# Performance work log

Hardware: AMD Instinct MI355X
Metric: run time of the kernel (lower is better)

## Reference

```python
import jax, jax.numpy as jnp
import numpy as np

B, C, T, H, HB, E, EH, TH = 512, 30, 3, 512, 512, 6, 512, 512
SCALE = 0.02
LOSS_COEF = 0.01


def setup_inputs() -> dict:
    key = jax.random.key(0)
    ks = jax.random.split(key, 12)
    return {
        "candidate_cls_embed": jax.random.normal(ks[0], (B, C, H), jnp.float32),
        "scores": jax.random.uniform(ks[1], (B, T, C), dtype=jnp.float32),
        "fc1_w": jax.random.normal(ks[2], (H, HB), jnp.float32) * SCALE,
        "fc1_b": jnp.zeros((HB,), jnp.float32),
        "fc2_w": jax.random.normal(ks[3], (HB, H), jnp.float32) * SCALE,
        "fc2_b": jnp.zeros((H,), jnp.float32),
        "w_gate": jax.random.normal(ks[4], (T, H, E), jnp.float32) * SCALE,
        "expert_w1": jax.random.normal(ks[5], (E, H, EH), jnp.float32) * SCALE,
        "expert_b1": jnp.zeros((E, EH), jnp.float32),
        "expert_w2": jax.random.normal(ks[6], (E, EH, H), jnp.float32) * SCALE,
        "expert_b2": jnp.zeros((E, H), jnp.float32),
        "tower_w1": jax.random.normal(ks[7], (T, H, TH), jnp.float32) * SCALE,
        "tower_b1": jnp.zeros((T, TH), jnp.float32),
        "tower_w2": jax.random.normal(ks[8], (T, TH), jnp.float32) * SCALE,
        "tower_b2": jnp.zeros((T,), jnp.float32),
        "k": 3,
    }


def reference(candidate_cls_embed, scores, fc1_w, fc1_b, fc2_w, fc2_b, w_gate,
              expert_w1, expert_b1, expert_w2, expert_b2,
              tower_w1, tower_b1, tower_w2, tower_b2, k):
    n_experts = w_gate.shape[-1]
    n_tasks = scores.shape[1]

    # labels: 1 where score hits the per-task max (non-differentiable construction)
    labels = jax.lax.stop_gradient(
        (scores == scores.max(axis=-1, keepdims=True)).astype(scores.dtype))  # [B,T,C]

    # shared bottom: fc2(relu(fc1(x)))
    h = jax.nn.relu(candidate_cls_embed @ fc1_w + fc1_b) @ fc2_w + fc2_b  # [B,C,H]

    # per-task top-k gating (MMoE style)
    glog = jnp.einsum('bch,the->btce', h, w_gate)                 # [B,T,C,E]
    topv, topi = jax.lax.top_k(glog, k)                           # [B,T,C,k]
    topg = jax.nn.softmax(topv, axis=-1)                          # softmax over kept experts
    gates = jnp.sum(topg[..., None] * jax.nn.one_hot(topi, n_experts, dtype=topg.dtype),
                    axis=-2)                                      # [B,T,C,E]

    # all-expert MLPs (dense over E; E is small)
    eh = jax.nn.relu(jnp.einsum('bch,ehf->bcef', h, expert_w1) + expert_b1)  # [B,C,E,EH]
    eo = jnp.einsum('bcef,efh->bceh', eh, expert_w2) + expert_b2             # [B,C,E,H]

    # gated combination per task
    y = jnp.einsum('btce,bceh->btch', gates, eo)                  # [B,T,C,H]

    # per-task towers -> one logit per candidate
    th = jax.nn.relu(jnp.einsum('btch,thf->btcf', y, tower_w1) + tower_b1[None, :, None, :])
    logits = jnp.einsum('btcf,tf->btc', th, tower_w2) + tower_b2[None, :, None]  # [B,T,C]

    # BCE-with-logits, mean over candidates, mean over tasks
    bce = jnp.maximum(logits, 0.0) - logits * labels + jnp.log1p(jnp.exp(-jnp.abs(logits)))
    task_loss = bce.mean(axis=-1).mean(axis=-1)                   # [B]

    # aux load-balancing loss: cv^2 of per-expert importance per sample/task
    imp = gates.sum(axis=2)                                       # [B,T,E]
    cv2 = imp.var(axis=-1) / (imp.mean(axis=-1) ** 2 + 1e-10)     # [B,T]
    aux = LOSS_COEF * cv2.sum(axis=-1)                            # [B]

    loss = (task_loss + aux).mean()
    return loss
```

## Files before the change

kernel.cpp:

```cpp
#include <hip/hip_runtime.h>
#include <hip/hip_bf16.h>
#include <cstdint>
#include <cstddef>

typedef unsigned short u16;
typedef unsigned char u8;
typedef long i64;
typedef __bf16 bf16x8 __attribute__((ext_vector_type(8)));
typedef float f32x4 __attribute__((ext_vector_type(4)));
typedef u16 u16x8 __attribute__((ext_vector_type(8)));
typedef u8 u8x16 __attribute__((ext_vector_type(16)));
typedef i64 i64x2 __attribute__((ext_vector_type(2)));

#define NROWS 15360
#define KDIM 512
#define BDIM 512
#define CDIM 30
#define TDIM 3
#define EDIM 6

typedef __attribute__((address_space(1))) const unsigned int gu32;
typedef __attribute__((address_space(3))) unsigned int lu32;

__device__ __forceinline__ void gload16(const void* g, void* l) {
  __builtin_amdgcn_global_load_lds((gu32*)g, (lu32*)l, 16, 0, 0);
}

__device__ __forceinline__ float bf2f(u16 u) {
  union { unsigned i; float f; } v; v.i = ((unsigned)u) << 16; return v.f;
}
__device__ __forceinline__ u16 f2bf(float f) {
  union { float f; unsigned i; } v; v.f = f;
  unsigned r = v.i + 0x7fffu + ((v.i >> 16) & 1u);
  return (u16)(r >> 16);
}
__device__ __forceinline__ u8 f2fp8_sw(float v) {
  union { float f; unsigned u; } x; x.f = v;
  unsigned s = (x.u >> 24) & 0x80;
  x.u &= 0x7fffffffu;
  if (x.f < 0.0009765625f) return (u8)s;
  if (x.f > 448.f) return (u8)(s | 0x7e);
  int e; float m = frexpf(x.f, &e);
  if (e < -5) {
    int qq = (int)(x.f * 512.f + 0.5f);
    return (u8)(s | qq);
  }
  int qq = (int)(m * 16.f + 0.5f);
  if (qq == 16) { qq = 8; e++; }
  int E = e + 6;
  if (E >= 16 || (E == 15 && qq - 8 == 7)) return (u8)(s | 0x7e);
  return (u8)(s | (E << 3) | (qq - 8));
}
__device__ __forceinline__ unsigned cvt2fp8(float a, float b) {
#if __has_builtin(__builtin_amdgcn_cvt_pk_fp8_f32)
  return (unsigned)__builtin_amdgcn_cvt_pk_fp8_f32(a, b, 0, false) & 0xffffu;
#else
  return (unsigned)f2fp8_sw(a) | ((unsigned)f2fp8_sw(b) << 8);
#endif
}
__device__ __forceinline__ int permpos(int j) {
  return ((j & 24) << 1) + ((j & 32) >> 2) + (j & 7);
}

__global__ __launch_bounds__(256) void prep_kernel(
    const float* __restrict__ X, u16* __restrict__ Xb,
    const float* __restrict__ fc1, const float* __restrict__ fc2,
    const float* __restrict__ ew1, const float* __restrict__ ew2,
    const float* __restrict__ tw1, u16* __restrict__ wt, u8* __restrict__ w2q,
    const float* __restrict__ wg, u16* __restrict__ WgT,
    float* __restrict__ logits) {
  int bid = blockIdx.x;
  if (bid < 3840) {
    int i = (bid * 256 + threadIdx.x) * 8;
    float4 a = *(const float4*)(X + i);
    float4 b = *(const float4*)(X + i + 4);
    u16x8 v;
    v[0] = f2bf(a.x); v[1] = f2bf(a.y); v[2] = f2bf(a.z); v[3] = f2bf(a.w);
    v[4] = f2bf(b.x); v[5] = f2bf(b.y); v[6] = f2bf(b.z); v[7] = f2bf(b.w);
    *(u16x8*)(Xb + i) = v;
  } else if (bid < 4928) {
    int id = bid - 3840;
    int mid = id >> 6, tile = id & 63;
    const float* src;
    if (mid == 0) src = fc1;
    else if (mid == 1) src = fc2;
    else if (mid < 8) src = ew1 + (size_t)(mid - 2) * 262144;
    else if (mid < 14) src = ew2 + (size_t)(mid - 8) * 262144;
    else src = tw1 + (size_t)(mid - 14) * 262144;
    int tr = (tile >> 3) * 64, tc = (tile & 7) * 64;
    __shared__ float t[64][65];
    int c = threadIdx.x & 63, r0 = threadIdx.x >> 6;
#pragma unroll
    for (int i = 0; i < 16; i++) {
      int r = r0 + i * 4;
      t[r][c] = src[(size_t)(tr + r) * 512 + tc + c];
    }
    __syncthreads();
    if (mid >= 8 && mid < 14) {
      u8* dq = w2q + (size_t)(mid - 8) * 262144;
      int pc = tr + permpos(c);
#pragma unroll
      for (int i = 0; i < 16; i++) {
        int r = r0 + i * 4;
        dq[(size_t)(tc + r) * 512 + pc] = (u8)(cvt2fp8(t[c][r] * 64.f, 0.f) & 0xff);
      }
    } else {
      u16* dst = wt + (size_t)mid * 262144;
#pragma unroll
      for (int i = 0; i < 16; i++) {
        int r = r0 + i * 4;
        dst[(size_t)(tc + r) * 512 + tr + c] = f2bf(t[c][r]);
      }
    }
  } else if (bid < 4960) {
    int col = bid - 4928;
    for (int k = threadIdx.x; k < 512; k += 256) {
      u16 v = 0;
      if (col < 18) {
        int t = col / 6, e = col % 6;
        v = f2bf(wg[(size_t)(t * 512 + k) * 6 + e]);
      }
      WgT[(size_t)col * 512 + k] = v;
    }
  } else {
    int i = (bid - 4960) * 1024 + threadIdx.x * 4;
    float4 z; z.x = 0.f; z.y = 0.f; z.z = 0.f; z.w = 0.f;
    *(float4*)(logits + i) = z;
  }
}

__global__ __launch_bounds__(512, 4) void gemm256(
    const u16* __restrict__ A,
    const u16* __restrict__ BT,
    const float* __restrict__ bias,
    u8* __restrict__ Cq,
    int nby) {
  int nwg = gridDim.x;
  int cpx = nwg >> 3;
  int bid = blockIdx.x;
  int swz = (bid & 7) * cpx + (bid >> 3);
  int bx = swz / nby, by = swz % nby;
  int brow = bx * 128, bcol = by * 256;

  __shared__ u16 SB[3][12288];

  int tid = threadIdx.x, lane = tid & 63, w = tid >> 6;
  int wm = w >> 2, wn = w & 3;
  int l = lane & 15, q = lane >> 4;

  int srow = tid >> 2;
  int sc = tid & 3;
  int srcc = sc ^ ((srow >> 1) & 3);
  const u16* AgR = A + (size_t)(brow + srow) * KDIM + srcc * 8;
  const u16* BgR0 = BT + (size_t)(bcol + srow) * KDIM + srcc * 8;
  const u16* BgR1 = BgR0 + 128 * KDIM;
  int lo = w * 512;

#define STAGE256(buf, kt)                              \
  do {                                                 \
    int _ko = (kt) * 32;                               \
    gload16(AgR + _ko, (buf) + lo);                    \
    gload16(BgR0 + _ko, (buf) + 4096 + lo);            \
    gload16(BgR1 + _ko, (buf) + 8192 + lo);            \
  } while (0)

  f32x4 zero; zero[0] = 0.f; zero[1] = 0.f; zero[2] = 0.f; zero[3] = 0.f;
  f32x4 acc[4][4];
#pragma unroll
  for (int m = 0; m < 4; m++)
#pragma unroll
    for (int n = 0; n < 4; n++) acc[m][n] = zero;

  int rca = q ^ ((l >> 1) & 3);
  int arow = wm * 64 + l;
  int bro = wn * 64 + l;

  STAGE256(SB[0], 0);
  STAGE256(SB[1], 1);
  asm volatile("s_waitcnt vmcnt(3)" ::: "memory");
  __builtin_amdgcn_s_barrier();

  u16 *bc = SB[0], *bn = SB[1], *bq = SB[2];
#pragma unroll
  for (int kt = 0; kt < 16; ++kt) {
    if (kt < 14) STAGE256(bq, kt + 2);
    bf16x8 bfv[4];
#pragma unroll
    for (int n = 0; n < 4; n++)
      bfv[n] = *(const bf16x8*)&bc[4096 + (bro + n * 16) * 32 + rca * 8];
    __builtin_amdgcn_s_setprio(1);
#pragma unroll
    for (int m = 0; m < 4; m++) {
      bf16x8 af = *(const bf16x8*)&bc[(arow + m * 16) * 32 + rca * 8];
#pragma unroll
      for (int n = 0; n < 4; n++)
        acc[m][n] = __builtin_amdgcn_mfma_f32_16x16x32_bf16(af, bfv[n], acc[m][n], 0, 0, 0);
    }
    __builtin_amdgcn_s_setprio(0);
    asm volatile("s_waitcnt lgkmcnt(0)" ::: "memory");
    if (kt < 14)
      asm volatile("s_waitcnt vmcnt(3)" ::: "memory");
    else
      asm volatile("s_waitcnt vmcnt(0)" ::: "memory");
    __builtin_amdgcn_s_barrier();
    u16* t_ = bc; bc = bn; bn = bq; bq = t_;
  }
#undef STAGE256

  int colL = wn * 64 + l;
  u8* S8 = (u8*)&SB[0][0];
  float bvs[4];
#pragma unroll
  for (int n = 0; n < 4; n++) bvs[n] = bias[bcol + colL + n * 16];
#pragma unroll
  for (int m = 0; m < 4; m++) {
    int rl = wm * 64 + m * 16 + q * 4;
#pragma unroll
    for (int n = 0; n < 4; n++) {
      int j = n * 16 + l;
      int pc = wn * 64 + permpos(j);
      float v0 = fmaxf(acc[m][n][0] + bvs[n], 0.f) * 16.f;
      float v1 = fmaxf(acc[m][n][1] + bvs[n], 0.f) * 16.f;
      float v2 = fmaxf(acc[m][n][2] + bvs[n], 0.f) * 16.f;
      float v3 = fmaxf(acc[m][n][3] + bvs[n], 0.f) * 16.f;
      unsigned p01 = cvt2fp8(v0, v1);
      unsigned p23 = cvt2fp8(v2, v3);
      S8[(rl + 0) * 264 + pc] = (u8)(p01 & 0xff);
      S8[(rl + 1) * 264 + pc] = (u8)(p01 >> 8);
      S8[(rl + 2) * 264 + pc] = (u8)(p23 & 0xff);
      S8[(rl + 3) * 264 + pc] = (u8)(p23 >> 8);
    }
  }
  __syncthreads();
  int row = tid >> 2, cc = tid & 3;
#pragma unroll
  for (int j = 0; j < 4; j++)
    *(u8x16*)&Cq[(size_t)(brow + row) * 3072 + bcol + cc * 64 + j * 16] =
        *(const u8x16*)&S8[row * 264 + cc * 64 + j * 16];
}

__global__ __launch_bounds__(256, 2) void gemm_w2c(
    const u8* __restrict__ eh,
    const u8* __restrict__ W2q,
    const float* __restrict__ eb2,
    const float* __restrict__ gates,
    u16* __restrict__ y) {
  int nwg = gridDim.x, cpx = nwg >> 3;
  int bid = blockIdx.x;
  int swz = (bid & 7) * cpx + (bid >> 3);
  int bx = swz >> 2, by = swz & 3;
  int brow = bx * 64, bcol = by * 128;

  __shared__ __align__(16) u8 SB8[3][12288];
  __shared__ u16 glds[64 * 18];

  int tid = threadIdx.x, lane = tid & 63, w = tid >> 6;
  int l = lane & 15, q = lane >> 4;

  for (int i = tid; i < 64 * 18; i += 256) {
    int r = i / 18, te = i % 18;
    int gr = brow + r, b = gr / CDIM, c = gr % CDIM;
    int t = te / 6, e = te % 6;
    glds[i] = f2bf(gates[((size_t)(b * TDIM + t) * CDIM + c) * EDIM + e]);
  }
  float b2all[2][6];
#pragma unroll
  for (int ni = 0; ni < 2; ni++) {
    int col = bcol + w * 32 + ni * 16 + l;
#pragma unroll
    for (int e = 0; e < 6; e++) b2all[ni][e] = eb2[e * 512 + col];
  }

  int srow = tid >> 2, sc = tid & 3;
  int scA = sc ^ (srow & 3);
  const u8* Ag = eh + (size_t)(brow + srow) * 3072 + scA * 16;
  const u8* Bg0 = W2q + (size_t)(bcol + srow) * 512 + scA * 16;
  const u8* Bg1 = Bg0 + (size_t)64 * 512;
  int lo = w * 1024;

#define STAGEW(buf, s2)                                                   \
  do {                                                                    \
    int _e2 = (s2) >> 3, _k2 = (s2) & 7;                                  \
    gload16(Ag + _e2 * 512 + _k2 * 64, (buf) + lo);                       \
    gload16(Bg0 + (size_t)_e2 * 262144 + _k2 * 64, (buf) + 4096 + lo);    \
    gload16(Bg1 + (size_t)_e2 * 262144 + _k2 * 64, (buf) + 8192 + lo);    \
  } while (0)

  f32x4 P[4][2], aY0[4][2], aY1[4][2], aY2[4][2];
#pragma unroll
  for (int mi = 0; mi < 4; mi++)
#pragma unroll
    for (int ni = 0; ni < 2; ni++) {
      P[mi][ni][0] = P[mi][ni][1] = P[mi][ni][2] = P[mi][ni][3] = 0.f;
      aY0[mi][ni] = P[mi][ni]; aY1[mi][ni] = P[mi][ni]; aY2[mi][ni] = P[mi][ni];
    }

  STAGEW(SB8[0], 0);
  STAGEW(SB8[1], 1);
  asm volatile("s_waitcnt vmcnt(3)" ::: "memory");
  __builtin_amdgcn_s_barrier();

  u8 *bc = SB8[0], *bn = SB8[1], *bq = SB8[2];
  for (int e = 0; e < 6; ++e) {
#pragma unroll
    for (int kt = 0; kt < 8; ++kt) {
      int s = e * 8 + kt;
      if (s < 46) STAGEW(bq, s + 2);
      i64x2 bfv[2], afv[4];
#pragma unroll
      for (int ni = 0; ni < 2; ni++) {
        int col = w * 32 + ni * 16 + l;
        bfv[ni] = *(const i64x2*)&bc[4096 + col * 64 + ((q ^ (col & 3)) * 16)];
      }
#pragma unroll
      for (int mi = 0; mi < 4; mi++) {
        int row = mi * 16 + l;
        afv[mi] = *(const i64x2*)&bc[row * 64 + ((q ^ (row & 3)) * 16)];
      }
      __builtin_amdgcn_s_setprio(1);
#pragma unroll
      for (int ks = 0; ks < 2; ++ks)
#pragma unroll
        for (int mi = 0; mi < 4; mi++)
#pragma unroll
          for (int ni = 0; ni < 2; ni++)
            P[mi][ni] = __builtin_amdgcn_mfma_f32_16x16x32_fp8_fp8(
                afv[mi][ks], bfv[ni][ks], P[mi][ni], 0, 0, 0);
      __builtin_amdgcn_s_setprio(0);
      asm volatile("s_waitcnt lgkmcnt(0)" ::: "memory");
      if (s < 46)
        asm volatile("s_waitcnt vmcnt(3)" ::: "memory");
      else
        asm volatile("s_waitcnt vmcnt(0)" ::: "memory");
      __builtin_amdgcn_s_barrier();
      u8* t_ = bc; bc = bn; bn = bq; bq = t_;
    }
#pragma unroll
    for (int mi = 0; mi < 4; mi++) {
#pragma unroll
      for (int rr = 0; rr < 4; rr++) {
        int row = mi * 16 + q * 4 + rr;
        float g0 = bf2f(glds[row * 18 + e]);
        float g1 = bf2f(glds[row * 18 + 6 + e]);
        float g2 = bf2f(glds[row * 18 + 12 + e]);
#pragma unroll
        for (int ni = 0; ni < 2; ni++) {
          float p = P[mi][ni][rr] * 9.765625e-4f + b2all[ni][e];
          aY0[mi][ni][rr] += g0 * p;
          aY1[mi][ni][rr] += g1 * p;
          aY2[mi][ni][rr] += g2 * p;
          P[mi][ni][rr] = 0.f;
        }
      }
    }
  }
#undef STAGEW

  u16* Sst = (u16*)&SB8[0][0];
#define EPI(AY, t)                                                          \
  do {                                                                      \
    _Pragma("unroll") for (int mi = 0; mi < 4; mi++)                        \
      _Pragma("unroll") for (int ni = 0; ni < 2; ni++)                      \
        _Pragma("unroll") for (int rr = 0; rr < 4; rr++)                    \
          Sst[(mi * 16 + q * 4 + rr) * 136 + w * 32 + ni * 16 + l] =        \
              f2bf(AY[mi][ni][rr]);                                         \
    __syncthreads();                                                        \
    {                                                                       \
      int row_ = tid >> 2, cc_ = tid & 3;                                   \
      _Pragma("unroll") for (int j = 0; j < 4; j++)                         \
        *(u16x8*)&y[((size_t)(t) * NROWS + brow + row_) * 512 + bcol +      \
                    cc_ * 32 + j * 8] =                                     \
            *(const u16x8*)&Sst[row_ * 136 + cc_ * 32 + j * 8];             \
    }                                                                       \
    __syncthreads();                                                        \
  } while (0)
  EPI(aY0, 0);
  EPI(aY1, 1);
  EPI(aY2, 2);
#undef EPI
}

__global__ __launch_bounds__(256, 2) void gemm_tower(
    const u16* __restrict__ yin, const u16* __restrict__ WTt,
    const float* __restrict__ tb1, const float* __restrict__ tw2,
    float* __restrict__ logits) {
  int t = blockIdx.z;
  const u16* A = yin + (size_t)t * NROWS * KDIM;
  const u16* BT = WTt + (size_t)t * 262144;
  const float* bias = tb1 + t * 512;

  __shared__ u16 Al[128 * 32];
  __shared__ u16 Bl[128 * 32];
  int tid = threadIdx.x, lane = tid & 63, w = tid >> 6;
  int wr = w >> 1, wc = w & 1;
  int brow = blockIdx.x * 128, bcol = blockIdx.y * 128;

  int srow = tid >> 2;
  int schunk = tid & 3;
  int srcc = schunk ^ ((srow >> 1) & 3);
  const u16* Ag0 = A + (size_t)(brow + srow) * KDIM + srcc * 8;
  const u16* Ag1 = A + (size_t)(brow + srow + 64) * KDIM + srcc * 8;
  const u16* Bg0 = BT + (size_t)(bcol + srow) * KDIM + srcc * 8;
  const u16* Bg1 = BT + (size_t)(bcol + srow + 64) * KDIM + srcc * 8;
  u16* Ald0 = Al + w * 512;
  u16* Ald1 = Al + 2048 + w * 512;
  u16* Bld0 = Bl + w * 512;
  u16* Bld1 = Bl + 2048 + w * 512;

  f32x4 zero; zero[0] = 0.f; zero[1] = 0.f; zero[2] = 0.f; zero[3] = 0.f;
  f32x4 acc[4][4];
#pragma unroll
  for (int m = 0; m < 4; m++)
#pragma unroll
    for (int n = 0; n < 4; n++) acc[m][n] = zero;

  int l = lane & 15, q = lane >> 4;
  int rc = q ^ ((l >> 1) & 3);
  int rbase = wr * 64 + l;
  int cbase = wc * 64 + l;

  for (int kt = 0; kt < 16; ++kt) {
    int ko = kt * 32;
    gload16(Ag0 + ko, Ald0);
    gload16(Ag1 + ko, Ald1);
    gload16(Bg0 + ko, Bld0);
    gload16(Bg1 + ko, Bld1);
    __syncthreads();
    bf16x8 af[4], bfr[4];
#pragma unroll
    for (int m = 0; m < 4; m++) af[m] = *(const bf16x8*)&Al[(rbase + m * 16) * 32 + rc * 8];
#pragma unroll
    for (int n = 0; n < 4; n++) bfr[n] = *(const bf16x8*)&Bl[(cbase + n * 16) * 32 + rc * 8];
#pragma unroll
    for (int m = 0; m < 4; m++)
#pragma unroll
      for (int n = 0; n < 4; n++)
        acc[m][n] = __builtin_amdgcn_mfma_f32_16x16x32_bf16(af[m], bfr[n], acc[m][n], 0, 0, 0);
    __syncthreads();
  }

  int col0 = bcol + wc * 64 + l;
  float bvs[4], tws[4];
#pragma unroll
  for (int n = 0; n < 4; n++) {
    int col = col0 + n * 16;
    bvs[n] = bias[col];
    tws[n] = tw2[t * 512 + col];
  }
  int row0 = brow + wr * 64 + q * 4;
#pragma unroll
  for (int m = 0; m < 4; m++) {
#pragma unroll
    for (int r = 0; r < 4; r++) {
      float s = 0.f;
#pragma unroll
      for (int n = 0; n < 4; n++) {
        float v = acc[m][n][r] + bvs[n];
        v = fmaxf(v, 0.f);
        s += v * tws[n];
      }
      s += __shfl_xor(s, 1, 64);
      s += __shfl_xor(s, 2, 64);
      s += __shfl_xor(s, 4, 64);
      s += __shfl_xor(s, 8, 64);
      if (l == 0) {
        int row = row0 + m * 16 + r;
        int b = row / CDIM, c = row % CDIM;
        atomicAdd(&logits[(size_t)(b * TDIM + t) * CDIM + c], s);
      }
    }
  }
}

template <int RELU>
__global__ __launch_bounds__(256, 2) void gemm_bt(
    const u16* __restrict__ A, int lda,
    const u16* __restrict__ BT,
    const float* __restrict__ bias,
    u16* __restrict__ C, int ldc) {
  __shared__ u16 S[8448];
  u16* Al = S;
  u16* Bl = S + 4096;
  int tid = threadIdx.x, lane = tid & 63, w = tid >> 6;
  int wr = w >> 1, wc = w & 1;
  int brow = blockIdx.x * 128, bcol = blockIdx.y * 128;

  int srow = tid >> 2;
  int schunk = tid & 3;
  int srcc = schunk ^ ((srow >> 1) & 3);
  const u16* Ag0 = A + (size_t)(brow + srow) * lda + srcc * 8;
  const u16* Ag1 = A + (size_t)(brow + srow + 64) * lda + srcc * 8;
  const u16* Bg0 = BT + (size_t)(bcol + srow) * KDIM + srcc * 8;
  const u16* Bg1 = BT + (size_t)(bcol + srow + 64) * KDIM + srcc * 8;
  u16* Ald0 = Al + w * 512;
  u16* Ald1 = Al + 2048 + w * 512;
  u16* Bld0 = Bl + w * 512;
  u16* Bld1 = Bl + 2048 + w * 512;

  f32x4 zero; zero[0] = 0.f; zero[1] = 0.f; zero[2] = 0.f; zero[3] = 0.f;
  f32x4 acc[4][4];
#pragma unroll
  for (int m = 0; m < 4; m++)
#pragma unroll
    for (int n = 0; n < 4; n++) acc[m][n] = zero;

  int l = lane & 15, q = lane >> 4;
  int rc = q ^ ((l >> 1) & 3);
  int rbase = wr * 64 + l;
  int cbase = wc * 64 + l;

  for (int kt = 0; kt < 16; ++kt) {
    int ko = kt * 32;
    gload16(Ag0 + ko, Ald0);
    gload16(Ag1 + ko, Ald1);
    gload16(Bg0 + ko, Bld0);
    gload16(Bg1 + ko, Bld1);
    __syncthreads();
    bf16x8 af[4], bfr[4];
#pragma unroll
    for (int m = 0; m < 4; m++) af[m] = *(const bf16x8*)&Al[(rbase + m * 16) * 32 + rc * 8];
#pragma unroll
    for (int n = 0; n < 4; n++) bfr[n] = *(const bf16x8*)&Bl[(cbase + n * 16) * 32 + rc * 8];
#pragma unroll
    for (int m = 0; m < 4; m++)
#pragma unroll
      for (int n = 0; n < 4; n++)
        acc[m][n] = __builtin_amdgcn_mfma_f32_16x16x32_bf16(af[m], bfr[n], acc[m][n], 0, 0, 0);
    __syncthreads();
  }

  int colL = wc * 64 + l;
  float bvs[4];
#pragma unroll
  for (int n = 0; n < 4; n++) bvs[n] = bias[bcol + colL + n * 16];
#pragma unroll
  for (int half = 0; half < 2; half++) {
    if (wr == half) {
#pragma unroll
      for (int m = 0; m < 4; m++) {
        int rl = m * 16 + q * 4;
#pragma unroll
        for (int n = 0; n < 4; n++) {
#pragma unroll
          for (int rr = 0; rr < 4; rr++) {
            float v = acc[m][n][rr] + bvs[n];
            if (RELU) v = fmaxf(v, 0.f);
            S[(rl + rr) * 132 + colL + n * 16] = f2bf(v);
          }
        }
      }
    }
    __syncthreads();
    int row = tid >> 2, cc = tid & 3;
#pragma unroll
    for (int j = 0; j < 4; j++)
      *(u16x8*)&C[(size_t)(brow + half * 64 + row) * ldc + bcol + cc * 32 + j * 8] =
          *(const u16x8*)&S[row * 132 + cc * 32 + j * 8];
    __syncthreads();
  }
}

__global__ __launch_bounds__(256) void gate_kernel(const u16* __restrict__ h,
                                                   const u16* __restrict__ WgT,
                                                   float* __restrict__ gates) {
  __shared__ u16 Wl[16 * 32 * 32];
  __shared__ float Gl[4][16][33];
  int tid = threadIdx.x, lane = tid & 63, w = tid >> 6;
  int l = lane & 15, q = lane >> 4;

  for (int idx = tid; idx < 2048; idx += 256) {
    int kt = idx >> 7, col = (idx >> 2) & 31, c = idx & 3;
    int sc = c ^ ((col >> 1) & 3);
    *(u16x8*)&Wl[kt * 1024 + col * 32 + c * 8] =
        *(const u16x8*)&WgT[(size_t)col * 512 + kt * 32 + sc * 8];
  }
  __syncthreads();

  int r = blockIdx.x * 64 + w * 16 + l;
  int ch = q ^ ((l >> 1) & 3);

  f32x4 acc0, acc1;
  acc0[0] = acc0[1] = acc0[2] = acc0[3] = 0.f;
  acc1 = acc0;
#pragma unroll
  for (int kt = 0; kt < 16; ++kt) {
    bf16x8 av = *(const bf16x8*)&h[(size_t)r * 512 + kt * 32 + q * 8];
    bf16x8 b0 = *(const bf16x8*)&Wl[kt * 1024 + l * 32 + ch * 8];
    bf16x8 b1 = *(const bf16x8*)&Wl[kt * 1024 + (16 + l) * 32 + ch * 8];
    acc0 = __builtin_amdgcn_mfma_f32_16x16x32_bf16(av, b0, acc0, 0, 0, 0);
    acc1 = __builtin_amdgcn_mfma_f32_16x16x32_bf16(av, b1, acc1, 0, 0, 0);
  }

#pragma unroll
  for (int rr = 0; rr < 4; rr++) {
    Gl[w][q * 4 + rr][l] = acc0[rr];
    Gl[w][q * 4 + rr][16 + l] = acc1[rr];
  }
  __syncthreads();

  if (lane < 16) {
    int R = blockIdx.x * 64 + w * 16 + lane;
    int b = R / CDIM, c = R % CDIM;
    for (int t = 0; t < 3; t++) {
      float g[6];
#pragma unroll
      for (int e = 0; e < 6; e++) g[e] = Gl[w][lane][t * 6 + e];
      float out[6] = {0, 0, 0, 0, 0, 0};
      int idx[3]; float val[3];
      unsigned used = 0;
      for (int kk = 0; kk < 3; kk++) {
        int best = 0; float bv = -1e30f;
        for (int e = 0; e < 6; e++)
          if (!((used >> e) & 1) && g[e] > bv) { bv = g[e]; best = e; }
        used |= 1u << best; idx[kk] = best; val[kk] = bv;
      }
      float mx = val[0];
      float s = 0.f, ex[3];
      for (int kk = 0; kk < 3; kk++) { ex[kk] = expf(val[kk] - mx); s += ex[kk]; }
      for (int kk = 0; kk < 3; kk++) out[idx[kk]] = ex[kk] / s;
      float* gp = &gates[(size_t)((b * TDIM + t) * CDIM + c) * EDIM];
      for (int e = 0; e < 6; e++) gp[e] = out[e];
    }
  }
}

__global__ __launch_bounds__(64) void loss_kernel(const float* __restrict__ scores,
                                                  const float* __restrict__ logits,
                                                  const float* __restrict__ gates,
                                                  const float* __restrict__ tb2,
                                                  float* __restrict__ out) {
  int b = blockIdx.x;
  int lane = threadIdx.x;
  float bce_sum = 0.f;
  float aux = 0.f;
  for (int t = 0; t < 3; t++) {
    float sc = (lane < CDIM) ? scores[(size_t)(b * TDIM + t) * CDIM + lane] : -1e30f;
    float mx = sc;
    for (int off = 32; off; off >>= 1) mx = fmaxf(mx, __shfl_xor(mx, off, 64));
    float lab = (lane < CDIM && sc == mx) ? 1.f : 0.f;
    float lg = (lane < CDIM) ? (logits[(size_t)(b * TDIM + t) * CDIM + lane] + tb2[t]) : 0.f;
    float bce = (lane < CDIM) ? (fmaxf(lg, 0.f) - lg * lab + log1pf(expf(-fabsf(lg)))) : 0.f;
    for (int off = 32; off; off >>= 1) bce += __shfl_xor(bce, off, 64);
    bce_sum += bce / (float)CDIM;

    float impv[6];
    float meansum = 0.f;
#pragma unroll
    for (int e = 0; e < 6; e++) {
      float gsum = (lane < CDIM) ? gates[(size_t)((b * TDIM + t) * CDIM + lane) * EDIM + e] : 0.f;
      for (int off = 32; off; off >>= 1) gsum += __shfl_xor(gsum, off, 64);
      impv[e] = gsum;
      meansum += gsum;
    }
    float mean = meansum / 6.f;
    float var = 0.f;
#pragma unroll
    for (int e = 0; e < 6; e++) { float d = impv[e] - mean; var += d * d; }
    var /= 6.f;
    aux += var / (mean * mean + 1e-10f);
  }
  float res = bce_sum / 3.f + 0.01f * aux;
  if (lane == 0) atomicAdd(out, res / (float)BDIM);
}

extern "C" void kernel_launch(void* const* d_in, const int* in_sizes, int n_in,
                              void* d_out, int out_size, void* d_ws, size_t ws_size,
                              hipStream_t stream) {
  const float* X = (const float*)d_in[0];
  const float* scores = (const float*)d_in[1];
  const float* fc1_w = (const float*)d_in[2];
  const float* fc1_b = (const float*)d_in[3];
  const float* fc2_w = (const float*)d_in[4];
  const float* fc2_b = (const float*)d_in[5];
  const float* w_gate = (const float*)d_in[6];
  const float* ew1 = (const float*)d_in[7];
  const float* eb1 = (const float*)d_in[8];
  const float* ew2 = (const float*)d_in[9];
  const float* eb2 = (const float*)d_in[10];
  const float* tw1 = (const float*)d_in[11];
  const float* tb1 = (const float*)d_in[12];
  const float* tw2 = (const float*)d_in[13];
  const float* tb2 = (const float*)d_in[14];
  float* out = (float*)d_out;

  u16* WT = (u16*)d_ws;
  u8* w2q = (u8*)(WT + (size_t)8 * 262144);
  u16* WgT = WT + (size_t)17 * 262144;
  u16* ehall = WgT + (size_t)32 * 512;
  u8* ehq = (u8*)ehall;
  u16* Xb = ehall + (size_t)NROWS * 1536;
  u16* A1 = Xb + (size_t)NROWS * 512;
  u16* h = ehall + (size_t)NROWS * 3072;
  u16* y = h + (size_t)NROWS * 512;
  float* gates = (float*)(y + (size_t)TDIM * NROWS * 512);
  float* logits = gates + (size_t)BDIM * TDIM * CDIM * EDIM;

  hipMemsetAsync(d_out, 0, sizeof(float) * out_size, stream);

  prep_kernel<<<5005, 256, 0, stream>>>(X, Xb, fc1_w, fc2_w, ew1, ew2, tw1, WT, w2q,
                                        w_gate, WgT, logits);

  gemm_bt<1><<<dim3(120, 4), 256, 0, stream>>>(Xb, 512, WT + (size_t)0 * 262144, fc1_b, A1, 512);
  gemm_bt<0><<<dim3(120, 4), 256, 0, stream>>>(A1, 512, WT + (size_t)1 * 262144, fc2_b, h, 512);

  gate_kernel<<<240, 256, 0, stream>>>(h, WgT, gates);

  gemm256<<<dim3(1440, 1, 1), 512, 0, stream>>>(h, WT + (size_t)2 * 262144, eb1, ehq, 12);

  gemm_w2c<<<dim3(960, 1, 1), 256, 0, stream>>>(ehq, w2q, eb2, gates, y);

  gemm_tower<<<dim3(120, 4, 3), 256, 0, stream>>>(y, WT + (size_t)14 * 262144, tb1, tw2, logits);

  loss_kernel<<<BDIM, 64, 0, stream>>>(scores, logits, gates, tb2, out);
}
```

Baseline: 245.3 us.

## Quantize tower GEMM to FP8 with FP8 y output and pipelined loads

The expert-combine kernel now writes the per-task y tensor as scaled FP8 instead of bf16. The tower weights are quantized to FP8 during prep. The tower GEMM is rewritten to use FP8 MFMA with a triple-buffered async load pipeline and a swizzled 64x128 tiling, and it rescales the result in the epilogue. This halves y write/read traffic and doubles MFMA throughput for the tower stage, at the cost of extra quantization error in the loss. The LDS swizzle in the expert kernel also changes to the (row>>1) pattern.

```diff
diff --git a/kernel.cpp b/kernel.cpp
--- a/kernel.cpp
+++ b/kernel.cpp
@@ -66,7 +66,8 @@
     const float* __restrict__ X, u16* __restrict__ Xb,
     const float* __restrict__ fc1, const float* __restrict__ fc2,
     const float* __restrict__ ew1, const float* __restrict__ ew2,
-    const float* __restrict__ tw1, u16* __restrict__ wt, u8* __restrict__ w2q,
+    const float* __restrict__ tw1, u16* __restrict__ wt,
+    u8* __restrict__ w2q, u8* __restrict__ tw1q,
     const float* __restrict__ wg, u16* __restrict__ WgT,
     float* __restrict__ logits) {
   int bid = blockIdx.x;
@@ -96,8 +97,9 @@
       t[r][c] = src[(size_t)(tr + r) * 512 + tc + c];
     }
     __syncthreads();
-    if (mid >= 8 && mid < 14) {
-      u8* dq = w2q + (size_t)(mid - 8) * 262144;
+    if (mid >= 8) {
+      u8* dq = (mid < 14) ? w2q + (size_t)(mid - 8) * 262144
+                          : tw1q + (size_t)(mid - 14) * 262144;
       int pc = tr + permpos(c);
 #pragma unroll
       for (int i = 0; i < 16; i++) {
@@ -244,7 +246,7 @@
     const u8* __restrict__ W2q,
     const float* __restrict__ eb2,
     const float* __restrict__ gates,
-    u16* __restrict__ y) {
+    u8* __restrict__ yq) {
   int nwg = gridDim.x, cpx = nwg >> 3;
   int bid = blockIdx.x;
   int swz = (bid & 7) * cpx + (bid >> 3);
@@ -272,9 +274,9 @@
   }
 
   int srow = tid >> 2, sc = tid & 3;
-  int scA = sc ^ (srow & 3);
-  const u8* Ag = eh + (size_t)(brow + srow) * 3072 + scA * 16;
-  const u8* Bg0 = W2q + (size_t)(bcol + srow) * 512 + scA * 16;
+  int scX = sc ^ ((srow >> 1) & 3);
+  const u8* Ag = eh + (size_t)(brow + srow) * 3072 + scX * 16;
+  const u8* Bg0 = W2q + (size_t)(bcol + srow) * 512 + scX * 16;
   const u8* Bg1 = Bg0 + (size_t)64 * 512;
   int lo = w * 1024;
 
@@ -295,6 +297,8 @@
       aY0[mi][ni] = P[mi][ni]; aY1[mi][ni] = P[mi][ni]; aY2[mi][ni] = P[mi][ni];
     }
 
+  int xg = q ^ ((l >> 1) & 3);
+
   STAGEW(SB8[0], 0);
   STAGEW(SB8[1], 1);
   asm volatile("s_waitcnt vmcnt(3)" ::: "memory");
@@ -310,12 +314,12 @@
 #pragma unroll
       for (int ni = 0; ni < 2; ni++) {
         int col = w * 32 + ni * 16 + l;
-        bfv[ni] = *(const i64x2*)&bc[4096 + col * 64 + ((q ^ (col & 3)) * 16)];
+        bfv[ni] = *(const i64x2*)&bc[4096 + col * 64 + xg * 16];
       }
 #pragma unroll
       for (int mi = 0; mi < 4; mi++) {
         int row = mi * 16 + l;
-        afv[mi] = *(const i64x2*)&bc[row * 64 + ((q ^ (row & 3)) * 16)];
+        afv[mi] = *(const i64x2*)&bc[row * 64 + xg * 16];
       }
       __builtin_amdgcn_s_setprio(1);
 #pragma unroll
@@ -356,21 +360,29 @@
   }
 #undef STAGEW
 
-  u16* Sst = (u16*)&SB8[0][0];
+  u8* S8 = (u8*)&SB8[0][0];
 #define EPI(AY, t)                                                          \
   do {                                                                      \
-    _Pragma("unroll") for (int mi = 0; mi < 4; mi++)                        \
-      _Pragma("unroll") for (int ni = 0; ni < 2; ni++)                      \
-        _Pragma("unroll") for (int rr = 0; rr < 4; rr++)                    \
-          Sst[(mi * 16 + q * 4 + rr) * 136 + w * 32 + ni * 16 + l] =        \
-              f2bf(AY[mi][ni][rr]);                                         \
+    _Pragma("unroll") for (int mi = 0; mi < 4; mi++) {                      \
+      int rl = mi * 16 + q * 4;                                             \
+      _Pragma("unroll") for (int ni = 0; ni < 2; ni++) {                    \
+        int colL = w * 32 + ni * 16 + l;                                    \
+        int pc = (colL & 64) + permpos(colL & 63);                          \
+        unsigned p01 = cvt2fp8(AY[mi][ni][0] * 32.f, AY[mi][ni][1] * 32.f); \
+        unsigned p23 = cvt2fp8(AY[mi][ni][2] * 32.f, AY[mi][ni][3] * 32.f); \
+        S8[(rl + 0) * 144 + pc] = (u8)(p01 & 0xff);                         \
+        S8[(rl + 1) * 144 + pc] = (u8)(p01 >> 8);                           \
+        S8[(rl + 2) * 144 + pc] = (u8)(p23 & 0xff);                         \
+        S8[(rl + 3) * 144 + pc] = (u8)(p23 >> 8);                           \
+      }                                                                     \
+    }                                                                       \
     __syncthreads();                                                        \
     {                                                                       \
       int row_ = tid >> 2, cc_ = tid & 3;                                   \
-      _Pragma("unroll") for (int j = 0; j < 4; j++)                         \
-        *(u16x8*)&y[((size_t)(t) * NROWS + brow + row_) * 512 + bcol +      \
-                    cc_ * 32 + j * 8] =                                     \
-            *(const u16x8*)&Sst[row_ * 136 + cc_ * 32 + j * 8];             \
+      _Pragma("unroll") for (int j = 0; j < 2; j++)                         \
+        *(u8x16*)&yq[((size_t)(t) * NROWS + brow + row_) * 512 + bcol +     \
+                     j * 64 + cc_ * 16] =                                   \
+            *(const u8x16*)&S8[row_ * 144 + j * 64 + cc_ * 16];             \
     }                                                                       \
     __syncthreads();                                                        \
   } while (0)
@@ -381,90 +393,113 @@
 }
 
 __global__ __launch_bounds__(256, 2) void gemm_tower(
-    const u16* __restrict__ yin, const u16* __restrict__ WTt,
+    const u8* __restrict__ yq,
+    const u8* __restrict__ tw1q,
     const float* __restrict__ tb1, const float* __restrict__ tw2,
     float* __restrict__ logits) {
   int t = blockIdx.z;
-  const u16* A = yin + (size_t)t * NROWS * KDIM;
-  const u16* BT = WTt + (size_t)t * 262144;
-  const float* bias = tb1 + t * 512;
-
-  __shared__ u16 Al[128 * 32];
-  __shared__ u16 Bl[128 * 32];
+  const u8* A = yq + (size_t)t * NROWS * 512;
+  const u8* BT = tw1q + (size_t)t * 262144;
+
+  int nwg = gridDim.x, cpx = nwg >> 3;
+  int bid = blockIdx.x;
+  int swz = (bid & 7) * cpx + (bid >> 3);
+  int bx = swz >> 2, by = swz & 3;
+  int brow = bx * 64, bcol = by * 128;
+
+  __shared__ __align__(16) u8 SB8[3][12288];
+
   int tid = threadIdx.x, lane = tid & 63, w = tid >> 6;
-  int wr = w >> 1, wc = w & 1;
-  int brow = blockIdx.x * 128, bcol = blockIdx.y * 128;
-
-  int srow = tid >> 2;
-  int schunk = tid & 3;
-  int srcc = schunk ^ ((srow >> 1) & 3);
-  const u16* Ag0 = A + (size_t)(brow + srow) * KDIM + srcc * 8;
-  const u16* Ag1 = A + (size_t)(brow + srow + 64) * KDIM + srcc * 8;
-  const u16* Bg0 = BT + (size_t)(bcol + srow) * KDIM + srcc * 8;
-  const u16* Bg1 = BT + (size_t)(bcol + srow + 64) * KDIM + srcc * 8;
-  u16* Ald0 = Al + w * 512;
-  u16* Ald1 = Al + 2048 + w * 512;
-  u16* Bld0 = Bl + w * 512;
-  u16* Bld1 = Bl + 2048 + w * 512;
-
-  f32x4 zero; zero[0] = 0.f; zero[1] = 0.f; zero[2] = 0.f; zero[3] = 0.f;
-  f32x4 acc[4][4];
-#pragma unroll
-  for (int m = 0; m < 4; m++)
-#pragma unroll
-    for (int n = 0; n < 4; n++) acc[m][n] = zero;
-
   int l = lane & 15, q = lane >> 4;
-  int rc = q ^ ((l >> 1) & 3);
-  int rbase = wr * 64 + l;
-  int cbase = wc * 64 + l;
-
-  for (int kt = 0; kt < 16; ++kt) {
-    int ko = kt * 32;
-    gload16(Ag0 + ko, Ald0);
-    gload16(Ag1 + ko, Ald1);
-    gload16(Bg0 + ko, Bld0);
-    gload16(Bg1 + ko, Bld1);
-    __syncthreads();
-    bf16x8 af[4], bfr[4];
-#pragma unroll
-    for (int m = 0; m < 4; m++) af[m] = *(const bf16x8*)&Al[(rbase + m * 16) * 32 + rc * 8];
-#pragma unroll
-    for (int n = 0; n < 4; n++) bfr[n] = *(const bf16x8*)&Bl[(cbase + n * 16) * 32 + rc * 8];
-#pragma unroll
-    for (int m = 0; m < 4; m++)
-#pragma unroll
-      for (int n = 0; n < 4; n++)
-        acc[m][n] = __builtin_amdgcn_mfma_f32_16x16x32_bf16(af[m], bfr[n], acc[m][n], 0, 0, 0);
-    __syncthreads();
-  }
-
-  int col0 = bcol + wc * 64 + l;
-  float bvs[4], tws[4];
-#pragma unroll
-  for (int n = 0; n < 4; n++) {
-    int col = col0 + n * 16;
-    bvs[n] = bias[col];
-    tws[n] = tw2[t * 512 + col];
-  }
-  int row0 = brow + wr * 64 + q * 4;
-#pragma unroll
-  for (int m = 0; m < 4; m++) {
-#pragma unroll
-    for (int r = 0; r < 4; r++) {
+
+  int srow = tid >> 2, sc = tid & 3;
+  int scX = sc ^ ((srow >> 1) & 3);
+  const u8* Ag = A + (size_t)(brow + srow) * 512 + scX * 16;
+  const u8* Bg0 = BT + (size_t)(bcol + srow) * 512 + scX * 16;
+  const u8* Bg1 = Bg0 + (size_t)64 * 512;
+  int lo = w * 1024;
+
+#define STAGET(buf, kt)                                \
+  do {                                                 \
+    gload16(Ag + (kt) * 64, (buf) + lo);               \
+    gload16(Bg0 + (kt) * 64, (buf) + 4096 + lo);       \
+    gload16(Bg1 + (kt) * 64, (buf) + 8192 + lo);       \
+  } while (0)
+
+  f32x4 P[4][2];
+#pragma unroll
+  for (int mi = 0; mi < 4; mi++)
+#pragma unroll
+    for (int ni = 0; ni < 2; ni++) {
+      P[mi][ni][0] = 0.f; P[mi][ni][1] = 0.f; P[mi][ni][2] = 0.f; P[mi][ni][3] = 0.f;
+    }
+
+  int xg = q ^ ((l >> 1) & 3);
+
+  STAGET(SB8[0], 0);
+  STAGET(SB8[1], 1);
+  asm volatile("s_waitcnt vmcnt(3)" ::: "memory");
+  __builtin_amdgcn_s_barrier();
+
+  u8 *bc = SB8[0], *bn = SB8[1], *bq = SB8[2];
+#pragma unroll
+  for (int kt = 0; kt < 8; ++kt) {
+    if (kt < 6) STAGET(bq, kt + 2);
+    i64x2 bfv[2], afv[4];
+#pragma unroll
+    for (int ni = 0; ni < 2; ni++) {
+      int col = w * 32 + ni * 16 + l;
+      bfv[ni] = *(const i64x2*)&bc[4096 + col * 64 + xg * 16];
+    }
+#pragma unroll
+    for (int mi = 0; mi < 4; mi++) {
+      int row = mi * 16 + l;
+      afv[mi] = *(const i64x2*)&bc[row * 64 + xg * 16];
+    }
+    __builtin_amdgcn_s_setprio(1);
+#pragma unroll
+    for (int ks = 0; ks < 2; ++ks)
+#pragma unroll
+      for (int mi = 0; mi < 4; mi++)
+#pragma unroll
+        for (int ni = 0; ni < 2; ni++)
+          P[mi][ni] = __builtin_amdgcn_mfma_f32_16x16x32_fp8_fp8(
+              afv[mi][ks], bfv[ni][ks], P[mi][ni], 0, 0, 0);
+    __builtin_amdgcn_s_setprio(0);
+    asm volatile("s_waitcnt lgkmcnt(0)" ::: "memory");
+    if (kt < 6)
+      asm volatile("s_waitcnt vmcnt(3)" ::: "memory");
+    else
+      asm volatile("s_waitcnt vmcnt(0)" ::: "memory");
+    __builtin_amdgcn_s_barrier();
+    u8* t_ = bc; bc = bn; bn = bq; bq = t_;
+  }
+#undef STAGET
+
+  float bvs[2], tws[2];
+#pragma unroll
+  for (int ni = 0; ni < 2; ni++) {
+    int col = bcol + w * 32 + ni * 16 + l;
+    bvs[ni] = tb1[t * 512 + col];
+    tws[ni] = tw2[t * 512 + col];
+  }
+#pragma unroll
+  for (int mi = 0; mi < 4; mi++) {
+#pragma unroll
+    for (int rr = 0; rr < 4; rr++) {
       float s = 0.f;
 #pragma unroll
-      for (int n = 0; n < 4; n++) {
-        float v = acc[m][n][r] + bvs[n];
+      for (int ni = 0; ni < 2; ni++) {
+        float v = P[mi][ni][rr] * 4.8828125e-4f + bvs[ni];
         v = fmaxf(v, 0.f);
-        s += v * tws[n];
+        s += v * tws[ni];
       }
       s += __shfl_xor(s, 1, 64);
       s += __shfl_xor(s, 2, 64);
       s += __shfl_xor(s, 4, 64);
       s += __shfl_xor(s, 8, 64);
       if (l == 0) {
-        int row = row0 + m * 16 + r;
+        int row = brow + mi * 16 + q * 4 + rr;
         int b = row / CDIM, c = row % CDIM;
         atomicAdd(&logits[(size_t)(b * TDIM + t) * CDIM + c], s);
       }
@@ -685,19 +720,20 @@
 
   u16* WT = (u16*)d_ws;
   u8* w2q = (u8*)(WT + (size_t)8 * 262144);
+  u8* tw1q = w2q + (size_t)6 * 262144;
   u16* WgT = WT + (size_t)17 * 262144;
   u16* ehall = WgT + (size_t)32 * 512;
   u8* ehq = (u8*)ehall;
   u16* Xb = ehall + (size_t)NROWS * 1536;
   u16* A1 = Xb + (size_t)NROWS * 512;
   u16* h = ehall + (size_t)NROWS * 3072;
-  u16* y = h + (size_t)NROWS * 512;
-  float* gates = (float*)(y + (size_t)TDIM * NROWS * 512);
+  u8* yq = (u8*)(h + (size_t)NROWS * 512);
+  float* gates = (float*)(yq + (size_t)TDIM * NROWS * 512);
   float* logits = gates + (size_t)BDIM * TDIM * CDIM * EDIM;
 
   hipMemsetAsync(d_out, 0, sizeof(float) * out_size, stream);
 
-  prep_kernel<<<5005, 256, 0, stream>>>(X, Xb, fc1_w, fc2_w, ew1, ew2, tw1, WT, w2q,
+  prep_kernel<<<5005, 256, 0, stream>>>(X, Xb, fc1_w, fc2_w, ew1, ew2, tw1, WT, w2q, tw1q,
                                         w_gate, WgT, logits);
 
   gemm_bt<1><<<dim3(120, 4), 256, 0, stream>>>(Xb, 512, WT + (size_t)0 * 262144, fc1_b, A1, 512);
@@ -707,9 +743,9 @@
 
   gemm256<<<dim3(1440, 1, 1), 512, 0, stream>>>(h, WT + (size_t)2 * 262144, eb1, ehq, 12);
 
-  gemm_w2c<<<dim3(960, 1, 1), 256, 0, stream>>>(ehq, w2q, eb2, gates, y);
-
-  gemm_tower<<<dim3(120, 4, 3), 256, 0, stream>>>(y, WT + (size_t)14 * 262144, tb1, tw2, logits);
+  gemm_w2c<<<dim3(960, 1, 1), 256, 0, stream>>>(ehq, w2q, eb2, gates, yq);
+
+  gemm_tower<<<dim3(960, 1, 3), 256, 0, stream>>>(yq, tw1q, tb1, tw2, logits);
 
   loss_kernel<<<BDIM, 64, 0, stream>>>(scores, logits, gates, tb2, out);
 }
```

New measurement: 236.0 us. 3.8% less time.
